# Performance work log

Measured on AMD Instinct MI355X. Metric: run time of the kernel, lower is better.

## Reference

```python
import jax, jax.numpy as jnp
import numpy as np

HIDDEN = 2048
H = 16            # num heads
Q_RANK = 1536
KV_RANK = 512
D_NOPE = 128
D_ROPE = 64
D_QK = D_NOPE + D_ROPE   # 192
D_V = 128
ROPE_BASE = 10000.0
EPS = 1e-6


def _rms_norm(x, w):
    xf = x.astype(jnp.float32)
    var = jnp.mean(xf * xf, axis=-1, keepdims=True)
    return w * (xf * jax.lax.rsqrt(var + EPS)).astype(x.dtype)


def _rotate_half(x):
    x1, x2 = x[..., : x.shape[-1] // 2], x[..., x.shape[-1] // 2:]
    return jnp.concatenate((-x2, x1), axis=-1)


def _rope_cos_sin(position_ids, dtype):
    inv_freq = 1.0 / (ROPE_BASE ** (jnp.arange(0, D_ROPE, 2, dtype=jnp.float32) / D_ROPE))
    freqs = position_ids.astype(jnp.float32)[..., None] * inv_freq  # [b,s,32]
    emb = jnp.concatenate((freqs, freqs), axis=-1)                  # [b,s,64]
    return jnp.cos(emb).astype(dtype), jnp.sin(emb).astype(dtype)


def setup_inputs() -> dict:
    key = jax.random.key(0)
    ks = jax.random.split(key, 8)
    b, s = 1, 2048
    scale = 0.02
    return {
        "hidden_states": jax.random.normal(ks[0], (b, s, HIDDEN), jnp.float32),
        "position_ids": jnp.broadcast_to(jnp.arange(s, dtype=jnp.int64)[None, :], (b, s)),
        "q_a_w": jax.random.normal(ks[1], (Q_RANK, HIDDEN), jnp.float32) * scale,
        "q_a_ln_w": jnp.ones((Q_RANK,), jnp.float32),
        "q_b_w": jax.random.normal(ks[2], (H * D_QK, Q_RANK), jnp.float32) * scale,
        "kv_a_w": jax.random.normal(ks[3], (KV_RANK + D_ROPE, HIDDEN), jnp.float32) * scale,
        "kv_a_ln_w": jnp.ones((KV_RANK,), jnp.float32),
        "kv_b_w": jax.random.normal(ks[4], (H * (D_NOPE + D_V), KV_RANK), jnp.float32) * scale,
        "o_w": jax.random.normal(ks[5], (HIDDEN, H * D_V), jnp.float32) * scale,
    }


def reference(hidden_states, position_ids, q_a_w, q_a_ln_w, q_b_w, kv_a_w, kv_a_ln_w, kv_b_w, o_w):
    b, s, _ = hidden_states.shape
    softmax_scale = D_QK ** (-0.5)

    # Q path: low-rank down-proj -> RMSNorm -> up-proj
    q_a = hidden_states @ q_a_w.T                              # [b,s,q_rank]
    q = (_rms_norm(q_a, q_a_ln_w) @ q_b_w.T).reshape(b, s, H, D_QK)
    q_nope, q_pe = q[..., :D_NOPE], q[..., D_NOPE:]

    # KV path: joint down-proj -> split latent / rope part
    kv_a = hidden_states @ kv_a_w.T                            # [b,s,kv_rank+rope]
    compressed_kv = _rms_norm(kv_a[..., :KV_RANK], kv_a_ln_w)  # [b,s,kv_rank]
    k_pe = kv_a[..., KV_RANK:]                                 # [b,s,rope]
    kv_b = (compressed_kv @ kv_b_w.T).reshape(b, s, H, D_NOPE + D_V)
    k_nope, v = kv_b[..., :D_NOPE], kv_b[..., D_NOPE:]

    # decoupled RoPE on the rope slice
    cos, sin = _rope_cos_sin(position_ids, hidden_states.dtype)  # [b,s,64]
    cos, sin = cos[:, :, None, :], sin[:, :, None, :]            # [b,s,1,64]
    q_pe = q_pe * cos + _rotate_half(q_pe) * sin                 # [b,s,H,64]
    k_pe_h = jnp.broadcast_to(k_pe[:, :, None, :], (b, s, H, D_ROPE))
    k_pe_h = k_pe_h * cos + _rotate_half(k_pe_h) * sin

    q_full = jnp.concatenate([q_nope, q_pe], axis=-1)            # [b,s,H,192]
    k_full = jnp.concatenate([k_nope, k_pe_h], axis=-1)          # [b,s,H,192]

    # naive materialized attention (matches reference)
    scores = jnp.einsum("bqhd,bkhd->bhqk", q_full, k_full) * softmax_scale
    causal = jnp.triu(jnp.full((s, s), -jnp.inf, dtype=scores.dtype), k=1)
    scores = scores + causal
    probs = jax.nn.softmax(scores.astype(jnp.float32), axis=-1).astype(q_full.dtype)
    attn = jnp.einsum("bhqk,bkhd->bqhd", probs, v).reshape(b, s, H * D_V)
    return attn @ o_w.T
```

## Files before the change

kernel.cpp:

```cpp
#include <hip/hip_runtime.h>
#include <stdint.h>

#define S_LEN 2048
#define HIDDEN_ 2048
#define NH 16
#define QR 1536
#define KVR 512
#define DN 128
#define DR 64
#define DQK 192
#define DV 128
#define NQKV 2112

#define KT_STRIDE 6144
#define VT_STRIDE 4096

typedef __attribute__((ext_vector_type(8))) short bf16x8;
typedef __attribute__((ext_vector_type(4))) float f32x4;
typedef __attribute__((ext_vector_type(4))) unsigned short u16x4;
typedef unsigned short u16;
typedef unsigned int u32;

#define GLOAD_LDS16(g, l)                                                      \
    __builtin_amdgcn_global_load_lds(                                          \
        (const __attribute__((address_space(1))) void*)(g),                    \
        (__attribute__((address_space(3))) void*)(l), 16, 0, 0)

__device__ inline float bf2f(u16 x) {
    union { u32 u; float f; } v; v.u = ((u32)x) << 16; return v.f;
}
__device__ inline u16 f2bf(float f) {
    union { float f; u32 u; } v; v.f = f;
    u32 u = v.u;
    return (u16)((u + 0x7fffu + ((u >> 16) & 1u)) >> 16);
}

__global__ void cvt3(const float* __restrict__ s0, u16* __restrict__ d0, int n0,
                     const float* __restrict__ s1, u16* __restrict__ d1, int n1,
                     const float* __restrict__ s2, u16* __restrict__ d2, int n2)
{
    const int b0 = n0 >> 10, b1 = n1 >> 10;
    int gid = blockIdx.x;
    const float* src; u16* dst; int base;
    if (gid < b0)           { src = s0; dst = d0; base = gid * 1024; }
    else if (gid < b0 + b1) { src = s1; dst = d1; base = (gid - b0) * 1024; }
    else                    { src = s2; dst = d2; base = (gid - b0 - b1) * 1024; }
    int i = base + threadIdx.x * 4;
    float4 v = *(const float4*)(src + i);
    u16x4 o;
    o[0] = f2bf(v.x); o[1] = f2bf(v.y); o[2] = f2bf(v.z); o[3] = f2bf(v.w);
    *(u16x4*)(dst + i) = o;
}

__device__ __forceinline__
void gemm_body(const u16* __restrict__ A, const u16* __restrict__ B,
               void* __restrict__ Cv, int M, int N, int Kloop, int ld,
               int out_f32, int bx, int by)
{
    __shared__ u16 sA[128 * 32];
    __shared__ u16 sB[128 * 32];
    const int tid  = threadIdx.x;
    const int wave = tid >> 6;
    const int lane = tid & 63;
    const int l16  = lane & 15;
    const int quad = lane >> 4;
    const int m_blk = by * 128;
    const int n_blk = bx * 128;
    const int wm = (wave >> 1) * 64;
    const int wn = (wave & 1) * 64;

    const f32x4 zero4 = {0.f, 0.f, 0.f, 0.f};
    f32x4 acc[4][4];
#pragma unroll
    for (int i = 0; i < 4; i++)
#pragma unroll
        for (int j = 0; j < 4; j++) acc[i][j] = zero4;

    const int srow = lane >> 2;
    const int scol = (lane & 3) * 8;

    for (int k0 = 0; k0 < Kloop; k0 += 32) {
        __syncthreads();
#pragma unroll
        for (int p = 0; p < 2; p++) {
            const int rbase = wave * 32 + p * 16;
            const int row = rbase + srow;
            const u16* ga = A + (size_t)(m_blk + row) * ld + k0 + scol;
            GLOAD_LDS16(ga, &sA[rbase * 32]);
            int brow = n_blk + row; if (brow >= N) brow = N - 1;
            const u16* gb = B + (size_t)brow * ld + k0 + scol;
            GLOAD_LDS16(gb, &sB[rbase * 32]);
        }
        __syncthreads();

        bf16x8 af[4], bfr[4];
#pragma unroll
        for (int i = 0; i < 4; i++)
            af[i] = *(const bf16x8*)(sA + (wm + i * 16 + l16) * 32 + quad * 8);
#pragma unroll
        for (int j = 0; j < 4; j++)
            bfr[j] = *(const bf16x8*)(sB + (wn + j * 16 + l16) * 32 + quad * 8);
#pragma unroll
        for (int i = 0; i < 4; i++)
#pragma unroll
            for (int j = 0; j < 4; j++)
                acc[i][j] = __builtin_amdgcn_mfma_f32_16x16x32_bf16(
                    af[i], bfr[j], acc[i][j], 0, 0, 0);
    }

#pragma unroll
    for (int i = 0; i < 4; i++)
#pragma unroll
        for (int j = 0; j < 4; j++)
#pragma unroll
            for (int r = 0; r < 4; r++) {
                int mrow = m_blk + wm + i * 16 + quad * 4 + r;
                int ncol = n_blk + wn + j * 16 + l16;
                if (ncol < N) {
                    if (out_f32)
                        ((float*)Cv)[(size_t)mrow * N + ncol] = acc[i][j][r];
                    else
                        ((u16*)Cv)[(size_t)mrow * N + ncol] = f2bf(acc[i][j][r]);
                }
            }
}

__global__ __launch_bounds__(256, 3)
void gemm1_fused(const u16* __restrict__ A, const u16* __restrict__ B,
                 float* __restrict__ C0, float* __restrict__ C1,
                 int M, int N, int Kh, int ld,
                 const float* s3, u16* d3, int n3,
                 const float* s4, u16* d4, int n4,
                 const float* s5, u16* d5, int n5)
{
    if (blockIdx.z < 2) {
        float* C = blockIdx.z ? C1 : C0;
        gemm_body(A + (size_t)blockIdx.z * Kh, B + (size_t)blockIdx.z * Kh,
                  C, M, N, Kh, ld, 1, blockIdx.x, blockIdx.y);
        return;
    }
    const int bid = blockIdx.y * gridDim.x + blockIdx.x;
    const int stride = gridDim.x * gridDim.y * 256 * 4;
    const int start = (bid * 256 + threadIdx.x) * 4;
    for (int i = start; i < n3; i += stride) {
        float4 v = *(const float4*)(s3 + i);
        u16x4 o; o[0]=f2bf(v.x); o[1]=f2bf(v.y); o[2]=f2bf(v.z); o[3]=f2bf(v.w);
        *(u16x4*)(d3 + i) = o;
    }
    for (int i = start; i < n4; i += stride) {
        float4 v = *(const float4*)(s4 + i);
        u16x4 o; o[0]=f2bf(v.x); o[1]=f2bf(v.y); o[2]=f2bf(v.z); o[3]=f2bf(v.w);
        *(u16x4*)(d4 + i) = o;
    }
    for (int i = start; i < n5; i += stride) {
        float4 v = *(const float4*)(s5 + i);
        u16x4 o; o[0]=f2bf(v.x); o[1]=f2bf(v.y); o[2]=f2bf(v.z); o[3]=f2bf(v.w);
        *(u16x4*)(d5 + i) = o;
    }
}

__global__ __launch_bounds__(256, 3)
void gemm_splitk(const u16* __restrict__ A, const u16* __restrict__ B,
                 float* __restrict__ C0, float* __restrict__ C1,
                 int M, int N, int Kh, int ld)
{
    float* C = blockIdx.z ? C1 : C0;
    gemm_body(A + (size_t)blockIdx.z * Kh, B + (size_t)blockIdx.z * Kh,
              C, M, N, Kh, ld, 1, blockIdx.x, blockIdx.y);
}

__global__ __launch_bounds__(256, 3)
void gemm_dual(const u16* A0, const u16* B0, u16* C0, int M0, int N0, int K0,
               const u16* A1, const u16* B1, u16* C1, int M1, int N1, int K1)
{
    if (blockIdx.z == 0) {
        if ((int)blockIdx.x >= (N0 + 127) / 128) return;
        gemm_body(A0, B0, C0, M0, N0, K0, K0, 0, blockIdx.x, blockIdx.y);
    } else {
        gemm_body(A1, B1, C1, M1, N1, K1, K1, 0, blockIdx.x, blockIdx.y);
    }
}

__global__ void rmsnorm2_k(const float* __restrict__ P0, const float* __restrict__ P1,
                           const float* __restrict__ W0, u16* __restrict__ Y0,
                           const float* __restrict__ W1, u16* __restrict__ Y1,
                           u16* __restrict__ kpe)
{
    const int row = blockIdx.x;
    const float* p0 = P0 + (size_t)row * NQKV;
    const float* p1 = P1 + (size_t)row * NQKV;
    __shared__ float xbuf[QR];
    __shared__ float red[4];
    int off, len; const float* W; u16* Y;
    if (blockIdx.y == 0) { off = 0;  len = QR;  W = W0; Y = Y0 + (size_t)row * QR;  }
    else                 { off = QR; len = KVR; W = W1; Y = Y1 + (size_t)row * KVR; }
    float ss = 0.f;
    for (int i = threadIdx.x; i < len; i += 256) {
        float v = p0[off + i] + p1[off + i];
        xbuf[i] = v;
        ss += v * v;
    }
#pragma unroll
    for (int o = 32; o; o >>= 1) ss += __shfl_down(ss, o, 64);
    if ((threadIdx.x & 63) == 0) red[threadIdx.x >> 6] = ss;
    __syncthreads();
    float tot = red[0] + red[1] + red[2] + red[3];
    float inv = 1.0f / sqrtf(tot / (float)len + 1e-6f);
    for (int i = threadIdx.x; i < len; i += 256)
        Y[i] = f2bf(W[i] * xbuf[i] * inv);
    if (blockIdx.y == 1 && threadIdx.x < DR) {
        int i = threadIdx.x;
        kpe[(size_t)row * DR + i] = f2bf(p0[QR + KVR + i] + p1[QR + KVR + i]);
    }
}

__global__ void repack_fused(const u16* __restrict__ q,
                             const u16* __restrict__ kvb,
                             const u16* __restrict__ kpe_b,
                             u16* __restrict__ Q, u16* __restrict__ Kf,
                             u16* __restrict__ Vt)
{
    __shared__ __align__(16) char smem[64 * 72 * 2];
    const int bid = blockIdx.x;
    const int t = threadIdx.x;

    if (bid < S_LEN) {
        float* cs = (float*)smem;
        float* sn = cs + 64;
        u16* kpe_r = (u16*)(sn + 64);
        const float QSC = 0.07216878364870323f * 1.4426950408889634f;
        const int s = bid;
        const float pos = (float)s;
        if (t < 64) {
            int jf = t & 31;
            float freq = powf(10000.f, -(float)(2 * jf) / 64.f);
            float ang = pos * freq;
            cs[t] = cosf(ang);
            sn[t] = sinf(ang);
        }
        __syncthreads();
        if (t < 64) {
            int j = t;
            float x = bf2f(kpe_b[(size_t)s * DR + j]);
            float other = (j < 32) ? -bf2f(kpe_b[(size_t)s * DR + j + 32])
                                   :  bf2f(kpe_b[(size_t)s * DR + j - 32]);
            kpe_r[j] = f2bf(x * cs[j] + other * sn[j]);
        }
        __syncthreads();

        for (int idx = t; idx < NH * 24; idx += 256) {
            const int h  = idx / 24;
            const int cg = idx % 24;
            const int d0v = cg * 8;
            const size_t qbase = (size_t)s * (NH * DQK) + h * DQK;
            bf16x8 qv, kv;
            if (d0v < DN) {
                bf16x8 qr = *(const bf16x8*)(q + qbase + d0v);
#pragma unroll
                for (int e = 0; e < 8; e++)
                    qv[e] = (short)f2bf(bf2f((u16)qr[e]) * QSC);
                kv = *(const bf16x8*)(kvb + (size_t)s * (NH * 256) + h * 256 + d0v);
            } else {
                const int j0 = d0v - DN;
#pragma unroll
                for (int e = 0; e < 8; e++) {
                    int j = j0 + e;
                    float x = bf2f(q[qbase + DN + j]);
                    float other = (j < 32) ? -bf2f(q[qbase + DN + j + 32])
                                           :  bf2f(q[qbase + DN + j - 32]);
                    qv[e] = (short)f2bf((x * cs[j] + other * sn[j]) * QSC);
                    kv[e] = (short)kpe_r[j];
                }
            }
            *(bf16x8*)&Q[((size_t)h * S_LEN + s) * DQK + d0v] = qv;
            const size_t koff = (size_t)(h * 64 + (s >> 5)) * KT_STRIDE
                              + (size_t)(cg * 32 + (s & 31)) * 8;
            *(bf16x8*)&Kf[koff] = kv;
        }
    } else {
        u16 (*tile)[72] = (u16(*)[72])smem;
        const int r   = bid - S_LEN;
        const int h   = r >> 6;
        const int rem = r & 63;
        const int s0  = (rem >> 1) * 64;
        const int d0  = (rem & 1) * 64;
#pragma unroll
        for (int p = 0; p < 2; p++) {
            int c = p * 256 + t;
            int rr = c >> 3, col = (c & 7) * 8;
            *(bf16x8*)&tile[rr][col] =
                *(const bf16x8*)&kvb[(size_t)(s0 + rr) * (NH * 256) + h * 256 + 128 + d0 + col];
        }
        __syncthreads();
#pragma unroll
        for (int p = 0; p < 2; p++) {
            int c = p * 256 + t;
            int dr = c >> 3, sc = (c & 7) * 8;
            bf16x8 v;
#pragma unroll
            for (int j = 0; j < 8; j++) v[j] = (short)tile[sc + j][dr];
            const int s_abs   = s0 + sc;
            const int kt      = s_abs >> 5;
            const int schunk  = (s_abs & 31) >> 3;
            const size_t voff = (size_t)(h * 64 + kt) * VT_STRIDE
                              + (size_t)(schunk * 128 + (d0 + dr)) * 8;
            *(bf16x8*)&Vt[voff] = v;
        }
    }
}

__global__ __launch_bounds__(256, 3)
void mla_attn(const u16* __restrict__ Q, const u16* __restrict__ Kf,
              const u16* __restrict__ Vt, u16* __restrict__ attn,
              float* __restrict__ part)
{
    const int lin = blockIdx.x + 48 * blockIdx.y;
    const int h   = ((lin & 7) << 1) | ((lin >> 3) & 1);
    const int bx  = lin >> 4;

    int s, tb, te, cIdx; bool direct;
    if (bx < 16)      { s = 16 + bx; tb = 0;  te = 32;        cIdx = 0; direct = false; }
    else if (bx < 32) { s = bx;      tb = 32; te = 2 * s + 2; cIdx = 1; direct = false; }
    else              { s = 47 - bx; tb = 0;  te = 2 * s + 2; cIdx = 0; direct = true;  }

    const int wave  = threadIdx.x >> 6;
    const int lane  = threadIdx.x & 63;
    const int l16   = lane & 15;
    const int quad  = lane >> 4;
    const int q0    = s * 64 + wave * 16;
    const int qrow  = q0 + l16;

    const u16* Qh  = Q  + (size_t)h * S_LEN * DQK;
    const u16* Kh  = Kf + (size_t)h * 64 * KT_STRIDE;
    const u16* Vth = Vt + (size_t)h * 64 * VT_STRIDE;

    __shared__ u16 sK[2][24 * 32 * 8];
    __shared__ u16 sV[2][4 * 128 * 8];

    bf16x8 qf[6];
#pragma unroll
    for (int st = 0; st < 6; st++)
        qf[st] = *(const bf16x8*)(Qh + (size_t)qrow * DQK + st * 32 + quad * 8);

    const f32x4 zero4 = {0.f, 0.f, 0.f, 0.f};
    f32x4 oacc[8];
#pragma unroll
    for (int t = 0; t < 8; t++) oacc[t] = zero4;
    float mrow = -INFINITY, lrow = 0.f;

    auto stage = [&](int buf, int kt) {
        const u16* kp = Kh + (size_t)kt * KT_STRIDE;
#pragma unroll
        for (int g = 0; g < 3; g++)
            GLOAD_LDS16(kp + (g * 256 + wave * 64 + lane) * 8,
                        &sK[buf][(g * 256 + wave * 64) * 8]);
        const u16* vp = Vth + (size_t)kt * VT_STRIDE;
#pragma unroll
        for (int g = 0; g < 2; g++)
            GLOAD_LDS16(vp + (g * 256 + wave * 64 + lane) * 8,
                        &sV[buf][(g * 256 + wave * 64) * 8]);
    };

    stage(0, tb);

    for (int kt = tb; kt < te; kt++) {
        const int c0  = kt * 32;
        const int cur = (kt - tb) & 1;
        __syncthreads();
        if (kt + 1 < te) stage(cur ^ 1, kt + 1);

        if (c0 <= q0 + 15) {
            f32x4 s0 = zero4, s1 = zero4;
            __builtin_amdgcn_s_setprio(1);
#pragma unroll
            for (int st = 0; st < 6; st++) {
                bf16x8 k0 = *(const bf16x8*)&sK[cur][((st * 4 + quad) * 32 + l16) * 8];
                bf16x8 k1 = *(const bf16x8*)&sK[cur][((st * 4 + quad) * 32 + 16 + l16) * 8];
                s0 = __builtin_amdgcn_mfma_f32_16x16x32_bf16(k0, qf[st], s0, 0, 0, 0);
                s1 = __builtin_amdgcn_mfma_f32_16x16x32_bf16(k1, qf[st], s1, 0, 0, 0);
            }
            __builtin_amdgcn_s_setprio(0);
            bf16x8 vfr[8];
#pragma unroll
            for (int t = 0; t < 8; t++)
                vfr[t] = *(const bf16x8*)&sV[cur][(quad * 128 + t * 16 + l16) * 8];

            const bool full = (c0 + 31 <= q0);
            float v0[4], v1[4];
#pragma unroll
            for (int r = 0; r < 4; r++) {
                v0[r] = s0[r];
                v1[r] = s1[r];
                if (!full) {
                    if (c0 + quad * 4 + r > qrow)      v0[r] = -INFINITY;
                    if (c0 + 16 + quad * 4 + r > qrow) v1[r] = -INFINITY;
                }
            }
            float lm = fmaxf(fmaxf(fmaxf(v0[0], v0[1]), fmaxf(v0[2], v0[3])),
                             fmaxf(fmaxf(v1[0], v1[1]), fmaxf(v1[2], v1[3])));
            lm = fmaxf(lm, __shfl_xor(lm, 16, 64));
            lm = fmaxf(lm, __shfl_xor(lm, 32, 64));

            float mref;
            if (__all(lm <= mrow + 11.5416f)) {
                mref = mrow;
            } else {
                mref = fmaxf(mrow, lm);
                const float alpha = __builtin_amdgcn_exp2f(mrow - mref);
#pragma unroll
                for (int t = 0; t < 8; t++) oacc[t] *= alpha;
                lrow *= alpha;
                mrow = mref;
            }

            float p0[4], p1[4], rs = 0.f;
#pragma unroll
            for (int r = 0; r < 4; r++) {
                p0[r] = __builtin_amdgcn_exp2f(v0[r] - mref);
                p1[r] = __builtin_amdgcn_exp2f(v1[r] - mref);
                rs += p0[r] + p1[r];
            }
            lrow += rs;

            u32 A0, A1, B0, B1;
            asm("v_cvt_pk_bf16_f32 %0, %1, %2" : "=v"(A0) : "v"(p0[0]), "v"(p0[1]));
            asm("v_cvt_pk_bf16_f32 %0, %1, %2" : "=v"(A1) : "v"(p0[2]), "v"(p0[3]));
            asm("v_cvt_pk_bf16_f32 %0, %1, %2" : "=v"(B0) : "v"(p1[0]), "v"(p1[1]));
            asm("v_cvt_pk_bf16_f32 %0, %1, %2" : "=v"(B1) : "v"(p1[2]), "v"(p1[3]));
            const int a0 = (((quad & 1) << 5) + l16) << 2;
            const int a1 = a0 + 64;
            u32 Y0 = (u32)__builtin_amdgcn_ds_bpermute(a0, (int)A0);
            u32 Y1 = (u32)__builtin_amdgcn_ds_bpermute(a0, (int)A1);
            u32 Y2 = (u32)__builtin_amdgcn_ds_bpermute(a1, (int)A0);
            u32 Y3 = (u32)__builtin_amdgcn_ds_bpermute(a1, (int)A1);
            u32 Z0 = (u32)__builtin_amdgcn_ds_bpermute(a0, (int)B0);
            u32 Z1 = (u32)__builtin_amdgcn_ds_bpermute(a0, (int)B1);
            u32 Z2 = (u32)__builtin_amdgcn_ds_bpermute(a1, (int)B0);
            u32 Z3 = (u32)__builtin_amdgcn_ds_bpermute(a1, (int)B1);
            const bool useA = quad < 2;
            union { u32 w[4]; bf16x8 v; } pf;
            pf.w[0] = useA ? Y0 : Z0;
            pf.w[1] = useA ? Y1 : Z1;
            pf.w[2] = useA ? Y2 : Z2;
            pf.w[3] = useA ? Y3 : Z3;
            bf16x8 pfrag = pf.v;

            __builtin_amdgcn_s_setprio(1);
#pragma unroll
            for (int t = 0; t < 8; t++)
                oacc[t] = __builtin_amdgcn_mfma_f32_16x16x32_bf16(vfr[t], pfrag,
                                                                  oacc[t], 0, 0, 0);
            __builtin_amdgcn_s_setprio(0);
        }
    }

    float lsum = lrow;
    lsum += __shfl_xor(lsum, 16, 64);
    lsum += __shfl_xor(lsum, 32, 64);

    if (direct) {
        const float linv = 1.0f / lsum;
#pragma unroll
        for (int t = 0; t < 8; t++) {
            u16x4 ov;
#pragma unroll
            for (int r = 0; r < 4; r++) ov[r] = f2bf(oacc[t][r] * linv);
            *(u16x4*)&attn[(size_t)qrow * (NH * DV) + h * DV + t * 16 + quad * 4] = ov;
        }
    } else {
        float* pout = part + ((size_t)(h * 16 + (s - 16)) * 2 + cIdx) * 8320;
        const int rowl = wave * 16 + l16;
#pragma unroll
        for (int t = 0; t < 8; t++) {
            float4 ov = {oacc[t][0], oacc[t][1], oacc[t][2], oacc[t][3]};
            *(float4*)&pout[(size_t)rowl * 128 + t * 16 + quad * 4] = ov;
        }
        if (quad == 0) {
            pout[8192 + rowl] = mrow;
            pout[8256 + rowl] = lsum;
        }
    }
}

__global__ void attn_combine(const float* __restrict__ part, u16* __restrict__ attn)
{
    const int h = blockIdx.y, sIdx = blockIdx.x;
    const int s = 16 + sIdx;
    const float* p0 = part + ((size_t)(h * 16 + sIdx) * 2 + 0) * 8320;
    const float* p1 = p0 + 8320;
    for (int e = threadIdx.x; e < 8192; e += 256) {
        int row = e >> 7, d = e & 127;
        float m0 = p0[8192 + row], m1 = p1[8192 + row];
        float l0 = p0[8256 + row], l1 = p1[8256 + row];
        float M  = fmaxf(m0, m1);
        float w0 = __builtin_amdgcn_exp2f(m0 - M);
        float w1 = __builtin_amdgcn_exp2f(m1 - M);
        float o  = (w0 * p0[e] + w1 * p1[e]) / (w0 * l0 + w1 * l1);
        attn[(size_t)(s * 64 + row) * (NH * DV) + h * DV + d] = f2bf(o);
    }
}

__global__ void addf2(const float* __restrict__ a, const float* __restrict__ b,
                      float* __restrict__ o, int n)
{
    int i = (blockIdx.x * 256 + threadIdx.x) * 4;
    if (i + 3 < n) {
        float4 va = *(const float4*)(a + i);
        float4 vb = *(const float4*)(b + i);
        float4 vo = {va.x + vb.x, va.y + vb.y, va.z + vb.z, va.w + vb.w};
        *(float4*)(o + i) = vo;
    }
}

extern "C" void kernel_launch(void* const* d_in, const int* in_sizes, int n_in,
                              void* d_out, int out_size, void* d_ws, size_t ws_size,
                              hipStream_t stream)
{
    const float* hid      = (const float*)d_in[0];
    const float* q_a_w    = (const float*)d_in[2];
    const float* q_a_ln_w = (const float*)d_in[3];
    const float* q_b_w    = (const float*)d_in[4];
    const float* kv_a_w   = (const float*)d_in[5];
    const float* kv_a_ln_w= (const float*)d_in[6];
    const float* kv_b_w   = (const float*)d_in[7];
    const float* o_w      = (const float*)d_in[8];

    char* base = (char*)d_ws;
    u16* qkvaw_b = (u16*)(base + 0);
    u16* qbw_b   = (u16*)(base + 8650752);
    u16* kvbw_b  = (u16*)(base + 18087936);
    u16* ow_b    = (u16*)(base + 22282240);
    u16* hid_b   = (u16*)(base + 30670848);
    float* P0    = (float*)(base + 39059456);
    float* P1    = (float*)(base + 56360960);
    u16* q_n     = (u16*)(base + 73662464);
    u16* ckv     = (u16*)(base + 79953920);
    u16* kpe_b   = (u16*)(base + 82051072);
    u16* qb      = (u16*)(base + 82313216);
    u16* kvb     = (u16*)(base + 94896128);
    u16* Qb      = (u16*)(base + 39059456);
    u16* Kb      = (u16*)(base + 51642368);
    u16* Vtb     = (u16*)(base + 64225280);
    u16* attnb   = (u16*)(base + 72613888);
    float* partb = (float*)(base + 94896128);
    float* PO0   = (float*)(base + 82313216);
    float* PO1   = (float*)(base + 99090432);

    cvt3<<<dim3(8320), 256, 0, stream>>>(
        hid,    hid_b,                          HIDDEN_ * S_LEN,
        q_a_w,  qkvaw_b,                        QR * HIDDEN_,
        kv_a_w, qkvaw_b + (size_t)QR * HIDDEN_, (KVR + DR) * HIDDEN_);

    gemm1_fused<<<dim3((NQKV + 127) / 128, S_LEN / 128, 3), 256, 0, stream>>>(
        hid_b, qkvaw_b, P0, P1, S_LEN, NQKV, HIDDEN_ / 2, HIDDEN_,
        q_b_w,  qbw_b,  NH * DQK * QR,
        kv_b_w, kvbw_b, NH * 256 * KVR,
        o_w,    ow_b,   HIDDEN_ * NH * DV);
    rmsnorm2_k<<<dim3(S_LEN, 2), 256, 0, stream>>>(
        P0, P1, q_a_ln_w, q_n, kv_a_ln_w, ckv, kpe_b);
    gemm_dual<<<dim3(32, S_LEN / 128, 2), 256, 0, stream>>>(
        q_n, qbw_b, qb,  S_LEN, NH * DQK, QR,
        ckv, kvbw_b, kvb, S_LEN, NH * 256, KVR);
    repack_fused<<<dim3(S_LEN + 1024), 256, 0, stream>>>(
        qb, kvb, kpe_b, Qb, Kb, Vtb);
    mla_attn<<<dim3(48, NH), 256, 0, stream>>>(Qb, Kb, Vtb, attnb, partb);
    attn_combine<<<dim3(16, NH), 256, 0, stream>>>(partb, attnb);
    gemm_splitk<<<dim3(HIDDEN_ / 128, S_LEN / 128, 2), 256, 0, stream>>>(
        attnb, ow_b, PO0, PO1, S_LEN, HIDDEN_, HIDDEN_ / 2, HIDDEN_);
    addf2<<<dim3((S_LEN * HIDDEN_) / 1024), 256, 0, stream>>>(
        PO0, PO1, (float*)d_out, S_LEN * HIDDEN_);
}
```

Measured before the change: 343.6 us.

## Redistribute weight conversions across kernels and add XCD-aware block swizzle to GEMMs

```diff
diff --git a/kernel.cpp b/kernel.cpp
--- a/kernel.cpp
+++ b/kernel.cpp
@@ -35,16 +35,33 @@
     return (u16)((u + 0x7fffu + ((u >> 16) & 1u)) >> 16);
 }
 
-__global__ void cvt3(const float* __restrict__ s0, u16* __restrict__ d0, int n0,
+__device__ inline void xcd_swz(int& bx, int& by, int& bz)
+{
+    const int gx = gridDim.x, gy = gridDim.y;
+    const int lin = blockIdx.x + gx * (blockIdx.y + gy * blockIdx.z);
+    const int q = (gx * gy * gridDim.z) >> 3;
+    const int swz = (lin & 7) * q + (lin >> 3);
+    bx = swz % gx;
+    const int t = swz / gx;
+    by = t % gy;
+    bz = t / gy;
+}
+
+__global__ void cvt5(const float* __restrict__ s0, u16* __restrict__ d0, int n0,
                      const float* __restrict__ s1, u16* __restrict__ d1, int n1,
-                     const float* __restrict__ s2, u16* __restrict__ d2, int n2)
-{
-    const int b0 = n0 >> 10, b1 = n1 >> 10;
+                     const float* __restrict__ s2, u16* __restrict__ d2, int n2,
+                     const float* __restrict__ s3, u16* __restrict__ d3, int n3,
+                     const float* __restrict__ s4, u16* __restrict__ d4, int n4)
+{
+    const int b0 = n0 >> 10, b1 = n1 >> 10, b2 = n2 >> 10, b3 = n3 >> 10;
     int gid = blockIdx.x;
     const float* src; u16* dst; int base;
-    if (gid < b0)           { src = s0; dst = d0; base = gid * 1024; }
-    else if (gid < b0 + b1) { src = s1; dst = d1; base = (gid - b0) * 1024; }
-    else                    { src = s2; dst = d2; base = (gid - b0 - b1) * 1024; }
+    if (gid < b0)                { src = s0; dst = d0; base = gid * 1024; }
+    else if (gid < b0 + b1)      { src = s1; dst = d1; base = (gid - b0) * 1024; }
+    else if (gid < b0 + b1 + b2) { src = s2; dst = d2; base = (gid - b0 - b1) * 1024; }
+    else if (gid < b0 + b1 + b2 + b3)
+                                 { src = s3; dst = d3; base = (gid - b0 - b1 - b2) * 1024; }
+    else                         { src = s4; dst = d4; base = (gid - b0 - b1 - b2 - b3) * 1024; }
     int i = base + threadIdx.x * 4;
     float4 v = *(const float4*)(src + i);
     u16x4 o;
@@ -126,58 +143,28 @@
 }
 
 __global__ __launch_bounds__(256, 3)
-void gemm1_fused(const u16* __restrict__ A, const u16* __restrict__ B,
-                 float* __restrict__ C0, float* __restrict__ C1,
-                 int M, int N, int Kh, int ld,
-                 const float* s3, u16* d3, int n3,
-                 const float* s4, u16* d4, int n4,
-                 const float* s5, u16* d5, int n5)
-{
-    if (blockIdx.z < 2) {
-        float* C = blockIdx.z ? C1 : C0;
-        gemm_body(A + (size_t)blockIdx.z * Kh, B + (size_t)blockIdx.z * Kh,
-                  C, M, N, Kh, ld, 1, blockIdx.x, blockIdx.y);
-        return;
-    }
-    const int bid = blockIdx.y * gridDim.x + blockIdx.x;
-    const int stride = gridDim.x * gridDim.y * 256 * 4;
-    const int start = (bid * 256 + threadIdx.x) * 4;
-    for (int i = start; i < n3; i += stride) {
-        float4 v = *(const float4*)(s3 + i);
-        u16x4 o; o[0]=f2bf(v.x); o[1]=f2bf(v.y); o[2]=f2bf(v.z); o[3]=f2bf(v.w);
-        *(u16x4*)(d3 + i) = o;
-    }
-    for (int i = start; i < n4; i += stride) {
-        float4 v = *(const float4*)(s4 + i);
-        u16x4 o; o[0]=f2bf(v.x); o[1]=f2bf(v.y); o[2]=f2bf(v.z); o[3]=f2bf(v.w);
-        *(u16x4*)(d4 + i) = o;
-    }
-    for (int i = start; i < n5; i += stride) {
-        float4 v = *(const float4*)(s5 + i);
-        u16x4 o; o[0]=f2bf(v.x); o[1]=f2bf(v.y); o[2]=f2bf(v.z); o[3]=f2bf(v.w);
-        *(u16x4*)(d5 + i) = o;
-    }
-}
-
-__global__ __launch_bounds__(256, 3)
 void gemm_splitk(const u16* __restrict__ A, const u16* __restrict__ B,
                  float* __restrict__ C0, float* __restrict__ C1,
                  int M, int N, int Kh, int ld)
 {
-    float* C = blockIdx.z ? C1 : C0;
-    gemm_body(A + (size_t)blockIdx.z * Kh, B + (size_t)blockIdx.z * Kh,
-              C, M, N, Kh, ld, 1, blockIdx.x, blockIdx.y);
+    int bx, by, bz;
+    xcd_swz(bx, by, bz);
+    float* C = bz ? C1 : C0;
+    gemm_body(A + (size_t)bz * Kh, B + (size_t)bz * Kh,
+              C, M, N, Kh, ld, 1, bx, by);
 }
 
 __global__ __launch_bounds__(256, 3)
 void gemm_dual(const u16* A0, const u16* B0, u16* C0, int M0, int N0, int K0,
                const u16* A1, const u16* B1, u16* C1, int M1, int N1, int K1)
 {
-    if (blockIdx.z == 0) {
-        if ((int)blockIdx.x >= (N0 + 127) / 128) return;
-        gemm_body(A0, B0, C0, M0, N0, K0, K0, 0, blockIdx.x, blockIdx.y);
+    int bx, by, bz;
+    xcd_swz(bx, by, bz);
+    if (bz == 0) {
+        if (bx >= (N0 + 127) / 128) return;
+        gemm_body(A0, B0, C0, M0, N0, K0, K0, 0, bx, by);
     } else {
-        gemm_body(A1, B1, C1, M1, N1, K1, K1, 0, blockIdx.x, blockIdx.y);
+        gemm_body(A1, B1, C1, M1, N1, K1, K1, 0, bx, by);
     }
 }
 
@@ -312,8 +299,20 @@
 __global__ __launch_bounds__(256, 3)
 void mla_attn(const u16* __restrict__ Q, const u16* __restrict__ Kf,
               const u16* __restrict__ Vt, u16* __restrict__ attn,
-              float* __restrict__ part)
-{
+              float* __restrict__ part,
+              const float* __restrict__ owf, u16* __restrict__ owb, int own)
+{
+    if (blockIdx.y == NH) {
+        const int stride = 48 * 256 * 4;
+        for (int i = (blockIdx.x * 256 + (int)threadIdx.x) * 4; i < own; i += stride) {
+            float4 v = *(const float4*)(owf + i);
+            u16x4 o;
+            o[0] = f2bf(v.x); o[1] = f2bf(v.y); o[2] = f2bf(v.z); o[3] = f2bf(v.w);
+            *(u16x4*)(owb + i) = o;
+        }
+        return;
+    }
+
     const int lin = blockIdx.x + 48 * blockIdx.y;
     const int h   = ((lin & 7) << 1) | ((lin >> 3) & 1);
     const int bx  = lin >> 4;
@@ -546,16 +545,15 @@
     float* PO0   = (float*)(base + 82313216);
     float* PO1   = (float*)(base + 99090432);
 
-    cvt3<<<dim3(8320), 256, 0, stream>>>(
+    cvt5<<<dim3(14976), 256, 0, stream>>>(
         hid,    hid_b,                          HIDDEN_ * S_LEN,
         q_a_w,  qkvaw_b,                        QR * HIDDEN_,
-        kv_a_w, qkvaw_b + (size_t)QR * HIDDEN_, (KVR + DR) * HIDDEN_);
-
-    gemm1_fused<<<dim3((NQKV + 127) / 128, S_LEN / 128, 3), 256, 0, stream>>>(
-        hid_b, qkvaw_b, P0, P1, S_LEN, NQKV, HIDDEN_ / 2, HIDDEN_,
-        q_b_w,  qbw_b,  NH * DQK * QR,
-        kv_b_w, kvbw_b, NH * 256 * KVR,
-        o_w,    ow_b,   HIDDEN_ * NH * DV);
+        kv_a_w, qkvaw_b + (size_t)QR * HIDDEN_, (KVR + DR) * HIDDEN_,
+        q_b_w,  qbw_b,                          NH * DQK * QR,
+        kv_b_w, kvbw_b,                         NH * 256 * KVR);
+
+    gemm_splitk<<<dim3((NQKV + 127) / 128, S_LEN / 128, 2), 256, 0, stream>>>(
+        hid_b, qkvaw_b, P0, P1, S_LEN, NQKV, HIDDEN_ / 2, HIDDEN_);
     rmsnorm2_k<<<dim3(S_LEN, 2), 256, 0, stream>>>(
         P0, P1, q_a_ln_w, q_n, kv_a_ln_w, ckv, kpe_b);
     gemm_dual<<<dim3(32, S_LEN / 128, 2), 256, 0, stream>>>(
@@ -563,7 +561,8 @@
         ckv, kvbw_b, kvb, S_LEN, NH * 256, KVR);
     repack_fused<<<dim3(S_LEN + 1024), 256, 0, stream>>>(
         qb, kvb, kpe_b, Qb, Kb, Vtb);
-    mla_attn<<<dim3(48, NH), 256, 0, stream>>>(Qb, Kb, Vtb, attnb, partb);
+    mla_attn<<<dim3(48, NH + 1), 256, 0, stream>>>(
+        Qb, Kb, Vtb, attnb, partb, o_w, ow_b, HIDDEN_ * NH * DV);
     attn_combine<<<dim3(16, NH), 256, 0, stream>>>(partb, attnb);
     gemm_splitk<<<dim3(HIDDEN_ / 128, S_LEN / 128, 2), 256, 0, stream>>>(
         attnb, ow_b, PO0, PO1, S_LEN, HIDDEN_, HIDDEN_ / 2, HIDDEN_);
```

Measured after the change: 354.6 us. 1.03x slower.
